# Optimization experiments

Measured on AMD Instinct MI355X. Metric: run time of the kernel, lower is better.

The kernel has to match this reference:

```python
import jax, jax.numpy as jnp
import numpy as np

RBF_BINS = 16
N_HEADS = 8
D_MODEL = 256
D_HEAD = D_MODEL // N_HEADS


def _rope(q, k):
    # q,k: [B,N,H,Dh]; standard rotate-half RoPE over the node dimension N
    B, N, H, Dh = q.shape
    inv_freq = 1.0 / (10000.0 ** (jnp.arange(0, Dh, 2, dtype=jnp.float32) / Dh))
    freqs = jnp.arange(N, dtype=jnp.float32)[:, None] * inv_freq[None, :]  # [N,Dh/2]
    emb = jnp.concatenate([freqs, freqs], axis=-1)  # [N,Dh]
    cos = jnp.cos(emb)[None, :, None, :].astype(q.dtype)
    sin = jnp.sin(emb)[None, :, None, :].astype(q.dtype)

    def rot_half(u):
        u1, u2 = jnp.split(u, 2, axis=-1)
        return jnp.concatenate([-u2, u1], axis=-1)

    return q * cos + rot_half(q) * sin, k * cos + rot_half(k) * sin


def _soft_one_hot(x, start, end, steps):
    xn = (x - start) / jnp.maximum(end - start, 1e-6)
    centers = jnp.linspace(0.0, 1.0, steps, dtype=x.dtype)
    width = 1.0 / (steps - 1 + 1e-9)
    d = jnp.abs(xn[..., None] - centers)
    return jnp.clip(1.0 - d / (width + 1e-9), 0.0)


def setup_inputs() -> dict:
    key = jax.random.key(0)
    ks = jax.random.split(key, 12)
    B, N = 2, 2048
    s = 1.0 / np.sqrt(D_MODEL)
    return {
        "x": jax.random.normal(ks[0], (B, N, D_MODEL), jnp.float32),
        "R": jax.random.normal(ks[1], (B, N, 3, 3), jnp.float32),
        "t": jax.random.normal(ks[2], (B, N, 3), jnp.float32),
        "node_mask": jnp.ones((B, N), dtype=bool),
        "Wq": jax.random.normal(ks[3], (D_MODEL, D_MODEL), jnp.float32) * s,
        "Wk": jax.random.normal(ks[4], (D_MODEL, D_MODEL), jnp.float32) * s,
        "Wv": jax.random.normal(ks[5], (D_MODEL, D_MODEL), jnp.float32) * s,
        "Wo": jax.random.normal(ks[6], (D_MODEL, D_MODEL), jnp.float32) * s,
        "W1": jax.random.normal(ks[7], (64, 20), jnp.float32) * (1.0 / np.sqrt(20)),
        "b1": jnp.zeros((64,), jnp.float32),
        "W2": jax.random.normal(ks[8], (N_HEADS, 64), jnp.float32) * 0.125,
        "b2": jnp.zeros((N_HEADS,), jnp.float32),
    }


def reference(x, R, t, node_mask, Wq, Wk, Wv, Wo, W1, b1, W2, b2):
    B, N, _ = x.shape
    q = (x @ Wq.T).reshape(B, N, N_HEADS, D_HEAD)
    k = (x @ Wk.T).reshape(B, N, N_HEADS, D_HEAD)
    q, k = _rope(q, k)
    v = (x @ Wv.T).reshape(B, N, N_HEADS, D_HEAD)
    scale = 1.0 / np.sqrt(D_HEAD)

    # pairwise displacement rotated into local frame i: e_local[b,i,j,:] = R[b,i]^T (t_j - t_i)
    delta = t[:, None, :, :] - t[:, :, None, :]  # [B,N(i),N(j),3]
    e_local = jnp.einsum('binm,bijn->bijm', R, delta)  # R^T applied
    r = jnp.maximum(jnp.linalg.norm(e_local, axis=-1), 1e-8)  # [B,N,N]
    ehat = e_local / r[..., None]
    r_end = jax.lax.stop_gradient(jnp.quantile(r, 0.95)) + 1e-6
    rbf = _soft_one_hot(r, 0.0, r_end, RBF_BINS)  # [B,N,N,16]
    geo = jnp.concatenate([r[..., None], ehat, rbf], axis=-1)  # [B,N,N,20]
    h = jax.nn.relu(geo @ W1.T + b1)
    bias = (h @ W2.T + b2)  # [B,N,N,H]
    bias = jnp.transpose(bias, (0, 1, 3, 2))  # [B,i,H,j]

    scores = jnp.einsum('bihd,bjhd->bihj', q, k) * scale + bias
    scores = jnp.where(node_mask[:, None, None, :], scores, -jnp.inf)
    attn = jax.nn.softmax(scores, axis=-1)
    out = jnp.einsum('bihj,bjhd->bihd', attn, v)
    out = out * node_mask[:, :, None, None].astype(out.dtype)
    y = out.reshape(B, N, N_HEADS * D_HEAD)
    return y @ Wo.T
```

## Files before the change

kernel.cpp:

```cpp
#include <hip/hip_runtime.h>
#include <hip/hip_bf16.h>
#include <math.h>

using bf16 = __hip_bfloat16;

#define B_ 2
#define N_ 2048
#define H_ 8
#define DH_ 32
#define D_ 256

typedef short bf16x8 __attribute__((ext_vector_type(8)));
typedef float f32x4  __attribute__((ext_vector_type(4)));

static __device__ __forceinline__ unsigned short f2bu(float v){
  bf16 b = __float2bfloat16(v);
  unsigned short u; __builtin_memcpy(&u, &b, 2); return u;
}
static __device__ __forceinline__ unsigned pk2(float lo, float hi){
  return __builtin_amdgcn_perm(__float_as_uint(hi) + 0x8000u,
                               __float_as_uint(lo) + 0x8000u, 0x07060302u);
}
static __device__ __forceinline__ unsigned pkw(float lo, float hi){
  return (unsigned)f2bu(lo) | ((unsigned)f2bu(hi) << 16);
}

__global__ __launch_bounds__(256) void k_prep(const float* __restrict__ x,
    const float* __restrict__ Wq, const float* __restrict__ Wk,
    const float* __restrict__ Wv, const float* __restrict__ Wo,
    unsigned short* __restrict__ xb, unsigned short* __restrict__ wb,
    float* __restrict__ cosT, float* __restrict__ sinT,
    unsigned* __restrict__ hist, unsigned* __restrict__ state){
  int bx = blockIdx.x, tid = threadIdx.x;
  if(bx < 1024){
    size_t g = (size_t)bx*256 + tid;
    float4 f = *(const float4*)(x + g*4);
    uint2 u; u.x = pk2(f.x, f.y); u.y = pk2(f.z, f.w);
    *(uint2*)(xb + g*4) = u;
  } else if(bx < 1280){
    int g = (bx - 1024)*256 + tid;
    int mat = g >> 14;
    int off = (g & 16383) * 4;
    const float* W = (mat==0)?Wq:(mat==1)?Wk:(mat==2)?Wv:Wo;
    float4 f = *(const float4*)(W + off);
    uint2 u; u.x = pkw(f.x, f.y); u.y = pkw(f.z, f.w);
    *(uint2*)(wb + (size_t)mat*65536 + off) = u;
  } else if(bx < 1408){
    int idx = (bx - 1280)*256 + tid;
    int n = idx >> 4, f = idx & 15;
    double invf = exp(-((double)(2*f)/32.0) * log(10000.0));
    double ang = (double)n * invf;
    cosT[idx] = (float)cos(ang);
    sinT[idx] = (float)sin(ang);
  } else {
    hist[(bx - 1408)*256 + tid] = 0u;
    if(bx == 1408 && tid == 0){ state[0] = 0u; state[1] = 7969177u; }
  }
}

__global__ __launch_bounds__(256) void k_gemm(const unsigned short* __restrict__ a_in,
    const unsigned short* __restrict__ wball, const float* __restrict__ cosT,
    const float* __restrict__ sinT, unsigned short* __restrict__ qb,
    unsigned short* __restrict__ kb, unsigned short* __restrict__ vtb,
    float* __restrict__ fout, int mode_base){
  __shared__ __align__(16) unsigned xs[64*132];
  int tid = threadIdx.x;
  int w = tid >> 6, lane = tid & 63, q = lane >> 4, c = lane & 15;
  int mode = mode_base + blockIdx.y;
  int row0 = blockIdx.x * 64;
  const unsigned short* wbm = wball + (size_t)((mode < 3) ? mode : 3)*65536;
  for(int e = tid; e < 2048; e += 256){
    int row = e >> 5, ch = e & 31;
    uint4 u = *(const uint4*)(a_in + (size_t)(row0+row)*256 + ch*8);
    *(uint4*)&xs[row*132 + ch*4] = u;
  }
  __syncthreads();
  f32x4 acc[4][4];
  #pragma unroll
  for(int a=0;a<4;a++)
    #pragma unroll
    for(int b2=0;b2<4;b2++) acc[a][b2] = (f32x4){0.f,0.f,0.f,0.f};
  for(int kk = 0; kk < 8; kk++){
    bf16x8 af[4], bfr[4];
    #pragma unroll
    for(int RT=0;RT<4;RT++) af[RT] = *(bf16x8*)&xs[(RT*16+c)*132 + kk*16 + q*4];
    #pragma unroll
    for(int CT=0;CT<4;CT++){
      int ocol = w*64 + CT*16 + c;
      bfr[CT] = *(const bf16x8*)(wbm + (size_t)ocol*256 + kk*32 + q*8);
    }
    #pragma unroll
    for(int RT=0;RT<4;RT++)
      #pragma unroll
      for(int CT=0;CT<4;CT++)
        acc[RT][CT] = __builtin_amdgcn_mfma_f32_16x16x32_bf16(af[RT], bfr[CT], acc[RT][CT], 0, 0, 0);
  }
  int bb = row0 >> 11, nloc0 = row0 & (N_-1);
  if(mode < 2){
    unsigned short* dst = (mode == 0) ? qb : kb;
    #pragma unroll
    for(int hp = 0; hp < 2; hp++){
      size_t bh = (size_t)bb*H_ + 2*w + hp;
      #pragma unroll
      for(int RT=0;RT<4;RT++)
        #pragma unroll
        for(int r=0;r<4;r++){
          int n = nloc0 + RT*16 + q*4 + r;
          float cs = cosT[n*16 + c], sn = sinT[n*16 + c];
          float d0 = acc[RT][hp*2][r], d1 = acc[RT][hp*2+1][r];
          float n0v = d0*cs - d1*sn;
          float n1v = d1*cs + d0*sn;
          float p0 = __shfl_xor(n0v, 1, 64);
          float p1 = __shfl_xor(n1v, 1, 64);
          if((c & 1) == 0){
            size_t idx = (bh*N_ + n)*32;
            *(unsigned*)(dst + idx + c)      = pk2(n0v, p0);
            *(unsigned*)(dst + idx + 16 + c) = pk2(n1v, p1);
          }
        }
    }
  } else if(mode == 2){
    #pragma unroll
    for(int CT=0;CT<4;CT++){
      int h = 2*w + (CT>>1), dh = (CT&1)*16 + c;
      size_t basev = ((size_t)(bb*H_ + h)*32 + dh)*N_;
      #pragma unroll
      for(int RT=0;RT<4;RT++){
        int n = nloc0 + RT*16 + q*4;
        uint2 u;
        u.x = pk2(acc[RT][CT][0], acc[RT][CT][1]);
        u.y = pk2(acc[RT][CT][2], acc[RT][CT][3]);
        *(uint2*)(vtb + basev + n) = u;
      }
    }
  } else {
    #pragma unroll
    for(int RT=0;RT<4;RT++)
      #pragma unroll
      for(int r=0;r<4;r++){
        size_t row = (size_t)row0 + RT*16 + q*4 + r;
        #pragma unroll
        for(int CT=0;CT<4;CT++)
          fout[row*256 + w*64 + CT*16 + c] = acc[RT][CT][r];
      }
  }
}

__global__ __launch_bounds__(256) void k_qh(const float* __restrict__ t_in,
    const float* __restrict__ R_in, const unsigned* __restrict__ state,
    unsigned* __restrict__ hist, int pass){
  __shared__ unsigned lh[4096];
  __shared__ float tl[N_][3];
  int tid = threadIdx.x;
  int row0 = blockIdx.x * 8;
  int b = row0 >> 11;
  for(int e = tid; e < 4096; e += 256) lh[e] = 0u;
  for(int e = tid; e < N_*3; e += 256) tl[e/3][e%3] = t_in[(size_t)b*N_*3 + e];
  __syncthreads();
  unsigned prefix = state[0];
  for(int rr = 0; rr < 8; rr++){
    int row = row0 + rr;
    int i = row & (N_-1);
    float tix = tl[i][0], tiy = tl[i][1], tiz = tl[i][2];
    float Rm[9];
    #pragma unroll
    for(int e=0;e<9;e++) Rm[e] = R_in[(size_t)row*9 + e];
    for(int j = tid; j < N_; j += 256){
      float dx = tl[j][0]-tix, dy = tl[j][1]-tiy, dz = tl[j][2]-tiz;
      float e0 = Rm[0]*dx + Rm[3]*dy + Rm[6]*dz;
      float e1 = Rm[1]*dx + Rm[4]*dy + Rm[7]*dz;
      float e2 = Rm[2]*dx + Rm[5]*dy + Rm[8]*dz;
      float r = fmaxf(sqrtf(e0*e0 + e1*e1 + e2*e2), 1e-8f);
      unsigned bits = __float_as_uint(r);
      if(pass == 0)
        atomicAdd(&lh[bits >> 20], 1u);
      else if((bits & 0xFFF00000u) == prefix)
        atomicAdd(&lh[(bits >> 8) & 4095u], 1u);
    }
  }
  __syncthreads();
  for(int e = tid; e < 4096; e += 256)
    if(lh[e]) atomicAdd(&hist[e], lh[e]);
}

__global__ void k_qs(unsigned* state, unsigned* hist, int shift, float* rend){
  __shared__ unsigned csum[256];
  int tid = threadIdx.x;
  unsigned local = 0;
  #pragma unroll
  for(int k = 0; k < 16; k++) local += hist[tid*16 + k];
  csum[tid] = local;
  __syncthreads();
  if(tid == 0){
    unsigned kr = state[1], cum = 0;
    int chunk = 255;
    for(int cc = 0; cc < 256; cc++){
      if(cum + csum[cc] > kr){ chunk = cc; break; }
      cum += csum[cc];
    }
    unsigned sel = (unsigned)chunk*16 + 15;
    for(int k = chunk*16; k < chunk*16 + 16; k++){
      unsigned c = hist[k];
      if(cum + c > kr){ sel = (unsigned)k; break; }
      cum += c;
    }
    state[1] = kr - cum;
    unsigned pre = state[0] | (sel << shift);
    state[0] = pre;
    if(shift == 8) *rend = __uint_as_float(pre) + 1e-6f;
  }
  __syncthreads();
  #pragma unroll
  for(int k = 0; k < 16; k++) hist[tid*16 + k] = 0u;
}

__global__ __launch_bounds__(256,5) void k_biasm(const float* __restrict__ t_in, const float* __restrict__ R_in,
    const float* __restrict__ W1, const float* __restrict__ b1,
    const float* __restrict__ W2, const float* __restrict__ b2,
    const float* __restrict__ rend_p, unsigned short* __restrict__ biasS, int qtr){
  __shared__ __align__(16) unsigned geo[5120];
  __shared__ __align__(16) unsigned hsc[2304];
  int tid = threadIdx.x;
  int wid = tid >> 6, lane = tid & 63, q = lane >> 4, c = lane & 15;
  int bx = blockIdx.x;
  int jh = bx >> 10;
  int b = (bx >> 9) & 1, iq = bx & 511;
  int i = qtr*512 + iq;
  int gi = b*N_ + i;
  const float* tp = t_in + (size_t)b*N_*3;

  union FU { bf16x8 v; unsigned u[4]; };
  FU a1[4];
  #pragma unroll
  for(int T=0;T<4;T++){
    int r0 = T*16 + c;
    float wv[8];
    #pragma unroll
    for(int jj=0;jj<8;jj++){
      int k = q*8 + jj;
      float val = 0.f;
      if(k < 20)       val = W1[r0*20 + k];
      else if(k == 20) val = b1[r0];
      wv[jj] = val;
    }
    a1[T].u[0]=pkw(wv[0],wv[1]); a1[T].u[1]=pkw(wv[2],wv[3]);
    a1[T].u[2]=pkw(wv[4],wv[5]); a1[T].u[3]=pkw(wv[6],wv[7]);
  }
  FU a2[2];
  #pragma unroll
  for(int fr=0;fr<2;fr++){
    float wv[8];
    #pragma unroll
    for(int jj=0;jj<8;jj++){
      int k = fr*32 + q*8 + jj;
      wv[jj] = (c < 8) ? W2[c*64 + k] : 0.f;
    }
    a2[fr].u[0]=pkw(wv[0],wv[1]); a2[fr].u[1]=pkw(wv[2],wv[3]);
    a2[fr].u[2]=pkw(wv[4],wv[5]); a2[fr].u[3]=pkw(wv[6],wv[7]);
  }
  f32x4 binit;
  #pragma unroll
  for(int r=0;r<4;r++) binit[r] = (q < 2) ? b2[q*4 + r] : 0.f;

  float Rm[9];
  #pragma unroll
  for(int e=0;e<9;e++) Rm[e] = R_in[(size_t)gi*9 + e];
  float tix = tp[i*3], tiy = tp[i*3+1], tiz = tp[i*3+2];
  float tx[4], ty[4], tz[4];
  #pragma unroll
  for(int ss=0; ss<4; ss++){
    int jj = jh*1024 + (wid*4 + ss)*64 + lane;
    tx[ss] = tp[jj*3]; ty[ss] = tp[jj*3+1]; tz[ss] = tp[jj*3+2];
  }
  float s15 = 15.0f / rend_p[0];
  int grow = (wid*64 + lane)*20;
  unsigned short* g16 = (unsigned short*)geo;
  uint4 zq = {0u,0u,0u,0u};
  *(uint2*)&geo[grow + 10] = make_uint2(0x00003F80u, 0u);
  *(uint4*)&geo[grow + 12] = zq;
  size_t orow = ((size_t)b*H_*512 + iq)*2048;

  for(int s = 0; s < 4; s++){
    int jb = jh*1024 + (wid*4 + s)*64;
    float dx = tx[s]-tix, dy = ty[s]-tiy, dz = tz[s]-tiz;
    float e0 = Rm[0]*dx + Rm[3]*dy + Rm[6]*dz;
    float e1 = Rm[1]*dx + Rm[4]*dy + Rm[7]*dz;
    float e2 = Rm[2]*dx + Rm[5]*dy + Rm[8]*dz;
    float d2 = e0*e0 + e1*e1 + e2*e2;
    float rr = fmaxf(sqrtf(d2), 1e-8f);
    float ir = __builtin_amdgcn_rcpf(rr);
    float pos = rr * s15;
    float m0f = floorf(pos);
    int   m0  = (int)m0f;
    float w1r = pos - m0f, w0r = 1.0f - w1r;
    uint4 z0; z0.x = pk2(rr, e0*ir); z0.y = pk2(e1*ir, e2*ir); z0.z = 0u; z0.w = 0u;
    *(uint4*)&geo[grow]     = z0;
    *(uint4*)&geo[grow + 4] = zq;
    *(uint2*)&geo[grow + 8] = make_uint2(0u, 0u);
    if(m0 <= 15) g16[grow*2 + 4 + m0] = f2bu(w0r);
    if(m0 <= 14) g16[grow*2 + 5 + m0] = f2bu(w1r);
    bf16x8 gf[4];
    #pragma unroll
    for(int tt = 0; tt < 4; tt++)
      gf[tt] = *(bf16x8*)&geo[(wid*64 + tt*16 + c)*20 + q*4];
    #pragma unroll
    for(int tt = 0; tt < 4; tt++){
      f32x4 d1[4];
      #pragma unroll
      for(int T=0;T<4;T++){
        d1[T] = (f32x4){0.f,0.f,0.f,0.f};
        d1[T] = __builtin_amdgcn_mfma_f32_16x16x32_bf16(a1[T].v, gf[tt], d1[T], 0, 0, 0);
      }
      #pragma unroll
      for(int T=0;T<4;T++){
        uint2 dw;
        dw.x = pk2(fmaxf(d1[T][0],0.f), fmaxf(d1[T][1],0.f));
        dw.y = pk2(fmaxf(d1[T][2],0.f), fmaxf(d1[T][3],0.f));
        *(uint2*)&hsc[wid*576 + c*36 + T*8 + q*2] = dw;
      }
      bf16x8 hb0 = *(bf16x8*)&hsc[wid*576 + c*36 + q*4];
      bf16x8 hb1 = *(bf16x8*)&hsc[wid*576 + c*36 + q*4 + 16];
      f32x4 dv = binit;
      dv = __builtin_amdgcn_mfma_f32_16x16x32_bf16(a2[0].v, hb0, dv, 0, 0, 0);
      dv = __builtin_amdgcn_mfma_f32_16x16x32_bf16(a2[1].v, hb1, dv, 0, 0, 0);
      if(q < 2){
        size_t col = orow + (size_t)(jb + tt*16 + c);
        #pragma unroll
        for(int r=0;r<4;r++)
          biasS[col + (size_t)(q*4 + r)*(512*2048)] = f2bu(dv[r]);
      }
    }
  }
}

__global__ __launch_bounds__(512) void k_attn_m(const unsigned short* __restrict__ qb,
    const unsigned short* __restrict__ kb, const unsigned short* __restrict__ vtb,
    const unsigned* __restrict__ biasU, unsigned short* __restrict__ ab, int qtr){
  __shared__ float osc[8][32][16];
  __shared__ float msc[8][16], lsc[8][16];
  __shared__ __align__(16) unsigned ptile[8][320];
  int tid = threadIdx.x;
  int w = tid >> 6, lane = tid & 63, q = lane >> 4, c = lane & 15;
  int bx = blockIdx.x;
  int tile = bx & 31, hh = (bx >> 5) & 7, b = bx >> 8;
  int iqq = tile*16;
  size_t bh = (size_t)b*H_ + hh;
  bf16x8 qfrag = *(const bf16x8*)(qb + (bh*N_ + (size_t)(qtr*512 + iqq + c))*32 + q*8);
  const unsigned short* kbase = kb + bh*N_*32;
  const unsigned short* vbase = vtb + bh*32*N_;
  const unsigned* bbase = biasU + (bh*512 + (size_t)(iqq + c))*1024;

  float m_i = -INFINITY, l_i = 0.f;
  f32x4 oA = {0.f,0.f,0.f,0.f}, oB = {0.f,0.f,0.f,0.f};
  const float SCALE = 0.17677669529663687f;

  int j0 = w*256;
  bf16x8 kf0 = *(const bf16x8*)(kbase + (size_t)(j0 + c)*32 + q*8);
  bf16x8 kf1 = *(const bf16x8*)(kbase + (size_t)(j0 + 16 + c)*32 + q*8);
  bf16x8 vfa = *(const bf16x8*)(vbase + (size_t)c*N_ + j0 + q*8);
  bf16x8 vfb = *(const bf16x8*)(vbase + (size_t)(16 + c)*N_ + j0 + q*8);
  uint2  bd0 = *(const uint2*)(bbase + (j0 >> 1) + q*2);
  uint2  bd1 = *(const uint2*)(bbase + ((j0 + 16) >> 1) + q*2);

  for(int cc = 0; cc < 8; cc++){
    bf16x8 ck0 = kf0, ck1 = kf1, cva = vfa, cvb = vfb;
    uint2 cb0 = bd0, cb1 = bd1;
    int jn = w*256 + ((cc + 1) & 7)*32;
    kf0 = *(const bf16x8*)(kbase + (size_t)(jn + c)*32 + q*8);
    kf1 = *(const bf16x8*)(kbase + (size_t)(jn + 16 + c)*32 + q*8);
    vfa = *(const bf16x8*)(vbase + (size_t)c*N_ + jn + q*8);
    vfb = *(const bf16x8*)(vbase + (size_t)(16 + c)*N_ + jn + q*8);
    bd0 = *(const uint2*)(bbase + (jn >> 1) + q*2);
    bd1 = *(const uint2*)(bbase + ((jn + 16) >> 1) + q*2);

    f32x4 s0 = {0.f,0.f,0.f,0.f}, s1 = {0.f,0.f,0.f,0.f};
    s0 = __builtin_amdgcn_mfma_f32_16x16x32_bf16(ck0, qfrag, s0, 0, 0, 0);
    s1 = __builtin_amdgcn_mfma_f32_16x16x32_bf16(ck1, qfrag, s1, 0, 0, 0);
    float sv[8];
    sv[0] = fmaf(s0[0], SCALE, __uint_as_float(cb0.x << 16));
    sv[1] = fmaf(s0[1], SCALE, __uint_as_float(cb0.x & 0xffff0000u));
    sv[2] = fmaf(s0[2], SCALE, __uint_as_float(cb0.y << 16));
    sv[3] = fmaf(s0[3], SCALE, __uint_as_float(cb0.y & 0xffff0000u));
    sv[4] = fmaf(s1[0], SCALE, __uint_as_float(cb1.x << 16));
    sv[5] = fmaf(s1[1], SCALE, __uint_as_float(cb1.x & 0xffff0000u));
    sv[6] = fmaf(s1[2], SCALE, __uint_as_float(cb1.y << 16));
    sv[7] = fmaf(s1[3], SCALE, __uint_as_float(cb1.y & 0xffff0000u));
    float cmax = sv[0];
    #pragma unroll
    for(int e=1;e<8;e++) cmax = fmaxf(cmax, sv[e]);
    cmax = fmaxf(cmax, __shfl_xor(cmax, 16, 64));
    cmax = fmaxf(cmax, __shfl_xor(cmax, 32, 64));
    float newm = fmaxf(m_i, cmax);
    float alpha = __expf(m_i - newm);
    float p[8], psum = 0.f;
    #pragma unroll
    for(int e=0;e<8;e++){ p[e] = __expf(sv[e] - newm); psum += p[e]; }
    psum += __shfl_xor(psum, 16, 64);
    psum += __shfl_xor(psum, 32, 64);
    l_i = l_i*alpha + psum;
    m_i = newm;
    #pragma unroll
    for(int r=0;r<4;r++){ oA[r] *= alpha; oB[r] *= alpha; }
    uint2 w0; w0.x = pk2(p[0], p[1]); w0.y = pk2(p[2], p[3]);
    uint2 w1; w1.x = pk2(p[4], p[5]); w1.y = pk2(p[6], p[7]);
    *(uint2*)&ptile[w][c*20 + q*2]     = w0;
    *(uint2*)&ptile[w][c*20 + 8 + q*2] = w1;
    bf16x8 pfrag = *(bf16x8*)&ptile[w][c*20 + q*4];
    oA = __builtin_amdgcn_mfma_f32_16x16x32_bf16(cva, pfrag, oA, 0, 0, 0);
    oB = __builtin_amdgcn_mfma_f32_16x16x32_bf16(cvb, pfrag, oB, 0, 0, 0);
  }
  if(q == 0){ msc[w][c] = m_i; lsc[w][c] = l_i; }
  #pragma unroll
  for(int r=0;r<4;r++){
    osc[w][q*4 + r][c]      = oA[r];
    osc[w][16 + q*4 + r][c] = oB[r];
  }
  __syncthreads();
  int mi = tid & 15, md = tid >> 4;
  float M = msc[0][mi];
  #pragma unroll
  for(int ww=1;ww<8;ww++) M = fmaxf(M, msc[ww][mi]);
  float L = 0.f, val = 0.f;
  #pragma unroll
  for(int ww=0;ww<8;ww++){
    float e = __expf(msc[ww][mi] - M);
    L += lsc[ww][mi]*e;
    val += osc[ww][md][mi]*e;
  }
  ab[((size_t)b*N_ + qtr*512 + iqq + mi)*D_ + hh*32 + md] = f2bu(val / L);
}

extern "C" void kernel_launch(void* const* d_in, const int* in_sizes, int n_in,
                              void* d_out, int out_size, void* d_ws, size_t ws_size,
                              hipStream_t stream){
  const float* x  = (const float*)d_in[0];
  const float* R  = (const float*)d_in[1];
  const float* t  = (const float*)d_in[2];
  const float* Wq = (const float*)d_in[4];
  const float* Wk = (const float*)d_in[5];
  const float* Wv = (const float*)d_in[6];
  const float* Wo = (const float*)d_in[7];
  const float* W1 = (const float*)d_in[8];
  const float* b1 = (const float*)d_in[9];
  const float* W2 = (const float*)d_in[10];
  const float* b2 = (const float*)d_in[11];
  float* out = (float*)d_out;

  char* base = (char*)d_ws;
  float* cosT = (float*)base;
  float* sinT = (float*)(base + (1u<<17));
  unsigned short* xb = (unsigned short*)(base + (1u<<18));
  unsigned short* wb = xb + (1u<<20);
  unsigned short* qbuf = wb + (1u<<18);
  unsigned short* kbuf = qbuf + (1u<<20);
  unsigned short* vtb  = kbuf + (1u<<20);
  unsigned short* ab   = vtb  + (1u<<20);
  char* tail = (char*)(ab + (1u<<20));
  unsigned* state = (unsigned*)tail;
  float*    rend  = (float*)(tail + 64);
  unsigned* hist  = (unsigned*)(tail + 256);
  unsigned* biasU = (unsigned*)(tail + 20480);

  k_prep<<<1424, 256, 0, stream>>>(x, Wq, Wk, Wv, Wo, xb, wb, cosT, sinT, hist, state);
  k_gemm<<<dim3(64,3), 256, 0, stream>>>(xb, wb, cosT, sinT, qbuf, kbuf, vtb, out, 0);
  k_qh<<<512, 256, 0, stream>>>(t, R, state, hist, 0);
  k_qs<<<1, 256, 0, stream>>>(state, hist, 20, rend);
  k_qh<<<512, 256, 0, stream>>>(t, R, state, hist, 1);
  k_qs<<<1, 256, 0, stream>>>(state, hist, 8, rend);
  for(int qtr = 0; qtr < 4; qtr++){
    k_biasm<<<2048, 256, 0, stream>>>(t, R, W1, b1, W2, b2, rend, (unsigned short*)biasU, qtr);
    k_attn_m<<<512, 512, 0, stream>>>(qbuf, kbuf, vtb, biasU, ab, qtr);
  }
  k_gemm<<<dim3(64,1), 256, 0, stream>>>(ab, wb, cosT, sinT, qbuf, kbuf, vtb, out, 3);
}
```

Measured before the change: 426.5 us.

## Merge per-quarter bias and attention launches into single full-size grids

When the workspace can hold all four bias slabs, the bias kernel and the attention kernel each run as one large grid covering all query quarters, replacing the four alternating launch pairs. This removes launch gaps and the small-grid tail effects of each quarter. The attention block index is also remapped so that batch and head vary fastest within a tile. The trade-off is four times the bias workspace (about 128MB) and the loss of L2 reuse of a freshly written bias slab between producer and consumer.

```diff
diff --git a/kernel.cpp b/kernel.cpp
--- a/kernel.cpp
+++ b/kernel.cpp
@@ -9,6 +9,7 @@
 #define H_ 8
 #define DH_ 32
 #define D_ 256
+#define QSLAB ((size_t)16*1024*1024)
 
 typedef short bf16x8 __attribute__((ext_vector_type(8)));
 typedef float f32x4  __attribute__((ext_vector_type(4)));
@@ -217,12 +218,15 @@
 __global__ __launch_bounds__(256,5) void k_biasm(const float* __restrict__ t_in, const float* __restrict__ R_in,
     const float* __restrict__ W1, const float* __restrict__ b1,
     const float* __restrict__ W2, const float* __restrict__ b2,
-    const float* __restrict__ rend_p, unsigned short* __restrict__ biasS, int qtr){
+    const float* __restrict__ rend_p, unsigned short* __restrict__ biasS, int qtr_p){
   __shared__ __align__(16) unsigned geo[5120];
   __shared__ __align__(16) unsigned hsc[2304];
   int tid = threadIdx.x;
   int wid = tid >> 6, lane = tid & 63, q = lane >> 4, c = lane & 15;
-  int bx = blockIdx.x;
+  int bxg = blockIdx.x;
+  int qtr = (qtr_p >= 0) ? qtr_p : (bxg >> 11);
+  if(qtr_p < 0) biasS += (size_t)(bxg >> 11) * QSLAB;
+  int bx = bxg & 2047;
   int jh = bx >> 10;
   int b = (bx >> 9) & 1, iq = bx & 511;
   int i = qtr*512 + iq;
@@ -335,14 +339,18 @@
 
 __global__ __launch_bounds__(512) void k_attn_m(const unsigned short* __restrict__ qb,
     const unsigned short* __restrict__ kb, const unsigned short* __restrict__ vtb,
-    const unsigned* __restrict__ biasU, unsigned short* __restrict__ ab, int qtr){
+    const unsigned* __restrict__ biasU, unsigned short* __restrict__ ab, int qtr_p){
   __shared__ float osc[8][32][16];
   __shared__ float msc[8][16], lsc[8][16];
   __shared__ __align__(16) unsigned ptile[8][320];
   int tid = threadIdx.x;
   int w = tid >> 6, lane = tid & 63, q = lane >> 4, c = lane & 15;
-  int bx = blockIdx.x;
-  int tile = bx & 31, hh = (bx >> 5) & 7, b = bx >> 8;
+  int bxg = blockIdx.x;
+  int qtr = (qtr_p >= 0) ? qtr_p : (bxg >> 9);
+  if(qtr_p < 0) biasU += (size_t)(bxg >> 9) * (QSLAB/2);
+  int bx = bxg & 511;
+  int bhid = bx & 15, tile = bx >> 4;
+  int hh = bhid & 7, b = bhid >> 3;
   int iqq = tile*16;
   size_t bh = (size_t)b*H_ + hh;
   bf16x8 qfrag = *(const bf16x8*)(qb + (bh*N_ + (size_t)(qtr*512 + iqq + c))*32 + q*8);
@@ -459,7 +467,9 @@
   unsigned* state = (unsigned*)tail;
   float*    rend  = (float*)(tail + 64);
   unsigned* hist  = (unsigned*)(tail + 256);
-  unsigned* biasU = (unsigned*)(tail + 20480);
+  unsigned short* biasS = (unsigned short*)(tail + 20480);
+  size_t used_base = (size_t)((char*)biasS - base);
+  bool full = ws_size >= used_base + 4*QSLAB*sizeof(unsigned short) + 4096;
 
   k_prep<<<1424, 256, 0, stream>>>(x, Wq, Wk, Wv, Wo, xb, wb, cosT, sinT, hist, state);
   k_gemm<<<dim3(64,3), 256, 0, stream>>>(xb, wb, cosT, sinT, qbuf, kbuf, vtb, out, 0);
@@ -467,9 +477,14 @@
   k_qs<<<1, 256, 0, stream>>>(state, hist, 20, rend);
   k_qh<<<512, 256, 0, stream>>>(t, R, state, hist, 1);
   k_qs<<<1, 256, 0, stream>>>(state, hist, 8, rend);
-  for(int qtr = 0; qtr < 4; qtr++){
-    k_biasm<<<2048, 256, 0, stream>>>(t, R, W1, b1, W2, b2, rend, (unsigned short*)biasU, qtr);
-    k_attn_m<<<512, 512, 0, stream>>>(qbuf, kbuf, vtb, biasU, ab, qtr);
+  if(full){
+    k_biasm<<<8192, 256, 0, stream>>>(t, R, W1, b1, W2, b2, rend, biasS, -1);
+    k_attn_m<<<2048, 512, 0, stream>>>(qbuf, kbuf, vtb, (unsigned*)biasS, ab, -1);
+  } else {
+    for(int qtr = 0; qtr < 4; qtr++){
+      k_biasm<<<2048, 256, 0, stream>>>(t, R, W1, b1, W2, b2, rend, biasS, qtr);
+      k_attn_m<<<512, 512, 0, stream>>>(qbuf, kbuf, vtb, (unsigned*)biasS, ab, qtr);
+    }
   }
   k_gemm<<<dim3(64,1), 256, 0, stream>>>(ab, wb, cosT, sinT, qbuf, kbuf, vtb, out, 3);
 }
```

Result: faster. 363.6 us (-14.7%).
